# Optimization experiments

Measured on AMD Instinct MI355X. Metric: run time of the kernel, lower is better.

The kernel has to match this reference:

```python
import jax, jax.numpy as jnp
import numpy as np

H = 8  # head_num

def setup_inputs() -> dict:
    key = jax.random.key(0)
    k1, k2, k3, k4, k5 = jax.random.split(key, 5)
    n, e = 4096, 128
    x = jax.random.normal(k1, (n, e), dtype=jnp.float32)
    # torch Linear weights stored here as [in, out]; scale ~ 1/sqrt(fan_in)
    w_qkv = jax.random.normal(k2, (e, e * 3 * H), dtype=jnp.float32) * (1.0 / np.sqrt(e))
    b_qkv = jax.random.normal(k3, (e * 3 * H,), dtype=jnp.float32) * 0.01
    w_proj = jax.random.normal(k4, (e * H, e), dtype=jnp.float32) * (1.0 / np.sqrt(e * H))
    b_proj = jax.random.normal(k5, (e,), dtype=jnp.float32) * 0.01
    return {"x": x, "w_qkv": w_qkv, "b_qkv": b_qkv, "w_proj": w_proj, "b_proj": b_proj}

def reference(x, w_qkv, b_qkv, w_proj, b_proj):
    n, e = x.shape
    # packed layout along output dim is (h, d, qkv) per rearrange 'n (h d qkv) -> qkv h n d'
    qkv = (x @ w_qkv + b_qkv).reshape(n, H, e, 3)          # [n, h, d, 3]
    q = jnp.transpose(qkv[..., 0], (1, 0, 2))              # [h, n, d]
    k = jnp.transpose(qkv[..., 1], (1, 0, 2))
    v = jnp.transpose(qkv[..., 2], (1, 0, 2))
    energy = jnp.einsum('hqd,hkd->hqk', q, k)              # [h, n, n]
    scaling = jnp.asarray(e, x.dtype) ** 0.5
    att = jax.nn.softmax(energy, axis=-1) / scaling        # post-softmax scale (as in source)
    out = jnp.einsum('hqk,hkd->hqd', att, v)               # [h, n, d]
    out = jnp.transpose(out, (1, 0, 2)).reshape(n, H * e)  # [n, h*d]
    return out @ w_proj + b_proj
```

## Files before the change

### kernel.cpp

```cpp
#include <hip/hip_runtime.h>
#include <hip/hip_fp16.h>


#define N_TOK 4096
#define DH 128
#define NH 8

#define EXP2F(x) __builtin_amdgcn_exp2f(x)

typedef _Float16 f16;
typedef __attribute__((ext_vector_type(8))) _Float16 f16x8;
typedef __attribute__((ext_vector_type(2))) __fp16 hf2;
typedef __attribute__((ext_vector_type(4))) float f32x4;

#define GLD16(gsrc, ldst) __builtin_amdgcn_global_load_lds( \
    (const __attribute__((address_space(1))) void*)(gsrc), \
    (__attribute__((address_space(3))) void*)(ldst), 16, 0, 0)

__global__ __launch_bounds__(256) void conv_weights(
    const float* __restrict__ w_proj, const float* __restrict__ w_qkv,
    const float* __restrict__ b_qkv,
    f16* __restrict__ wpT, f16* __restrict__ wqkvT, float* __restrict__ bperm)
{
  int t = blockIdx.x * 256 + threadIdx.x;
  if (t < 131072) {
    int k = t >> 7, col = t & 127;
    wpT[col * 1024 + k] = (f16)w_proj[t];
  } else {
    t -= 131072;
    int k = t / 3072;
    int col = t - k * 3072;
    int hh = col / 384;
    int rem = col - hh * 384;
    int d = rem / 3;
    int s = rem - d * 3;
    int colp = s * 1024 + hh * 128 + d;
    float scale = (s == 0) ? 1.4426950408889634f : 1.0f;
    wqkvT[colp * 128 + k] = (f16)(w_qkv[t] * scale);
    if (k == 0) bperm[colp] = b_qkv[col] * scale;
  }
}

__global__ __launch_bounds__(256) void qkv_gemm2(
    const float* __restrict__ x, const f16* __restrict__ wqkvT,
    const float* __restrict__ bperm,
    f16* __restrict__ Qh, f16* __restrict__ Kh, f16* __restrict__ Vt)
{
  const int cb = blockIdx.x;
  const int rb = blockIdx.y;
  const int tid = threadIdx.x;
  const int w = tid >> 6, lane = tid & 63;
  const int l16 = lane & 15, lhi = lane >> 4;
  const int s = cb >> 3, h = cb & 7;

  f16x8 xf[2][4];
#pragma unroll
  for (int m = 0; m < 2; ++m)
#pragma unroll
    for (int kt = 0; kt < 4; ++kt) {
      const float* xp = x + (size_t)(rb * 128 + w * 32 + m * 16 + l16) * 128 + kt * 32 + lhi * 8;
      f32x4 x0 = *(const f32x4*)xp, x1 = *(const f32x4*)(xp + 4);
      f16x8 v;
#pragma unroll
      for (int j = 0; j < 4; ++j) { v[j] = (f16)x0[j]; v[4 + j] = (f16)x1[j]; }
      xf[m][kt] = v;
    }

  f32x4 acc[8][2];
#pragma unroll
  for (int nt = 0; nt < 8; ++nt)
#pragma unroll
    for (int m = 0; m < 2; ++m) acc[nt][m] = (f32x4){0.f, 0.f, 0.f, 0.f};

#pragma unroll
  for (int nt = 0; nt < 8; ++nt)
#pragma unroll
    for (int kt = 0; kt < 4; ++kt) {
      f16x8 wf = *(const f16x8*)(wqkvT + (size_t)(cb * 128 + nt * 16 + l16) * 128 + kt * 32 + lhi * 8);
      acc[nt][0] = __builtin_amdgcn_mfma_f32_16x16x32_f16(wf, xf[0][kt], acc[nt][0], 0, 0, 0);
      acc[nt][1] = __builtin_amdgcn_mfma_f32_16x16x32_f16(wf, xf[1][kt], acc[nt][1], 0, 0, 0);
    }

#pragma unroll
  for (int nt = 0; nt < 8; ++nt) {
    f32x4 bb = *(const f32x4*)(bperm + cb * 128 + nt * 16 + 4 * lhi);
#pragma unroll
    for (int m = 0; m < 2; ++m) acc[nt][m] += bb;
  }

  if (s == 2) {
#pragma unroll
    for (int nt = 0; nt < 8; ++nt)
#pragma unroll
      for (int m = 0; m < 2; ++m)
#pragma unroll
        for (int r = 0; r < 4; ++r)
          Vt[(size_t)(h * 128 + nt * 16 + 4 * lhi + r) * N_TOK + rb * 128 + w * 32 + m * 16 + l16] =
              (f16)acc[nt][m][r];
  } else {
    __shared__ f16 tr[128][136];
#pragma unroll
    for (int nt = 0; nt < 8; ++nt)
#pragma unroll
      for (int m = 0; m < 2; ++m)
#pragma unroll
        for (int r = 0; r < 4; ++r)
          tr[w * 32 + m * 16 + l16][nt * 16 + 4 * lhi + r] = (f16)acc[nt][m][r];
    __syncthreads();
    f16* dst = (s == 0 ? Qh : Kh) + (size_t)(h * N_TOK + rb * 128) * 128;
    int r = tid >> 1, dh = (tid & 1) * 64;
#pragma unroll
    for (int i = 0; i < 8; ++i)
      *(f16x8*)(dst + r * 128 + dh + i * 8) = *(const f16x8*)(&tr[r][dh + i * 8]);
  }
}

__global__ __launch_bounds__(256, 3) void flash_attn(
    const f16* __restrict__ Qh, const f16* __restrict__ Kh,
    const f16* __restrict__ Vt, f16* __restrict__ opart, float* __restrict__ mlpart)
{
  const int bid = blockIdx.x;
  const int h = bid & 7;
  const int rem8 = bid >> 3;
  const int sp = rem8 % 3, qb = rem8 / 3;
  const int tid = threadIdx.x;
  const int w = tid >> 6, lane = tid & 63;
  const int l16 = lane & 15, lhi = lane >> 4;

  __shared__ __align__(16) char smem[32768];

  f16x8 qf[2][4];
#pragma unroll
  for (int m = 0; m < 2; ++m)
#pragma unroll
    for (int kt = 0; kt < 4; ++kt)
      qf[m][kt] = *(const f16x8*)(Qh +
          (size_t)(h * N_TOK + qb * 128 + w * 32 + m * 16 + l16) * DH + kt * 32 + lhi * 8);

  int koff[4][4], voff[2][8];
#pragma unroll
  for (int nt = 0; nt < 4; ++nt) {
    int row = 32 * (nt >> 1) + 8 * (l16 >> 2) + 4 * (nt & 1) + (l16 & 3);
    int fk = (row & 3) | ((row & 8) >> 1);
#pragma unroll
    for (int kt = 0; kt < 4; ++kt)
      koff[nt][kt] = row * 256 + ((kt * 4 + lhi) ^ fk) * 16;
  }
#pragma unroll
  for (int ks = 0; ks < 2; ++ks)
#pragma unroll
    for (int dt = 0; dt < 8; ++dt) {
      int rowv = dt * 16 + l16;
      voff[ks][dt] = rowv * 128 + (((ks * 4 + lhi) ^ (rowv & 7))) * 16;
    }

  f32x4 o[2][8];
#pragma unroll
  for (int m = 0; m < 2; ++m)
#pragma unroll
    for (int dt = 0; dt < 8; ++dt) o[m][dt] = (f32x4){0.f, 0.f, 0.f, 0.f};
  float mrun[2] = {-3e38f, -3e38f}, lrun[2] = {0.f, 0.f};

  const f16* Kgh = Kh + (size_t)h * N_TOK * DH;
  const f16* Vgh = Vt + (size_t)h * DH * N_TOK;

  auto stage = [&](int kb) {
    char* kd = smem;
    char* vd = smem + 16384;
#pragma unroll
    for (int c4 = 0; c4 < 4; ++c4) {
      int c = w * 4 + c4;
      {
        int row = c * 4 + (lane >> 4);
        int fk = (row & 3) | ((row & 8) >> 1);
        const f16* src = Kgh + (size_t)(kb * 64 + row) * DH + ((lane & 15) ^ fk) * 8;
        GLD16(src, kd + c * 1024);
      }
      {
        int row = c * 8 + (lane >> 3);
        const f16* src = Vgh + (size_t)row * N_TOK + kb * 64 + ((lane & 7) ^ (row & 7)) * 8;
        GLD16(src, vd + c * 1024);
      }
    }
  };

  const int kb0 = (sp * 64) / 3;
  const int kb1 = ((sp + 1) * 64) / 3;
  const char* kd = smem;
  const char* vd = smem + 16384;

  for (int kb = kb0; kb < kb1; ++kb) {
    stage(kb);
    __syncthreads();

    f32x4 sv[2][4];
    __builtin_amdgcn_s_setprio(1);
#pragma unroll
    for (int nt = 0; nt < 4; ++nt) {
      f32x4 a0 = {0.f, 0.f, 0.f, 0.f}, a1 = {0.f, 0.f, 0.f, 0.f};
#pragma unroll
      for (int kt = 0; kt < 4; ++kt) {
        f16x8 kf = *(const f16x8*)(kd + koff[nt][kt]);
        a0 = __builtin_amdgcn_mfma_f32_16x16x32_f16(kf, qf[0][kt], a0, 0, 0, 0);
        a1 = __builtin_amdgcn_mfma_f32_16x16x32_f16(kf, qf[1][kt], a1, 0, 0, 0);
      }
      sv[0][nt] = a0; sv[1][nt] = a1;
    }
    __builtin_amdgcn_s_setprio(0);

    f16x8 pf[2][2];
#pragma unroll
    for (int m = 0; m < 2; ++m) {
      f32x4 mv;
#pragma unroll
      for (int r = 0; r < 4; ++r)
        mv[r] = fmaxf(fmaxf(sv[m][0][r], sv[m][1][r]), fmaxf(sv[m][2][r], sv[m][3][r]));
      float pmax = fmaxf(fmaxf(mv[0], mv[1]), fmaxf(mv[2], mv[3]));
      if (!__all(pmax - mrun[m] <= 8.f)) {
        float rm = fmaxf(pmax, __shfl_xor(pmax, 16));
        rm = fmaxf(rm, __shfl_xor(rm, 32));
        float mnew = fmaxf(mrun[m], rm);
        float sc = EXP2F(mrun[m] - mnew);
        lrun[m] *= sc;
#pragma unroll
        for (int dt = 0; dt < 8; ++dt) o[m][dt] *= sc;
        mrun[m] = mnew;
      }
      float mr = mrun[m];
      f32x4 ps = {0.f, 0.f, 0.f, 0.f};
#pragma unroll
      for (int nt = 0; nt < 4; ++nt)
#pragma unroll
        for (int r = 0; r < 4; ++r) {
          float p = EXP2F(sv[m][nt][r] - mr);
          sv[m][nt][r] = p;
          ps[r] += p;
        }
      lrun[m] += (ps[0] + ps[1]) + (ps[2] + ps[3]);
#pragma unroll
      for (int ks = 0; ks < 2; ++ks) {
        union { f16x8 v; hf2 hh[4]; } u;
        u.hh[0] = __builtin_amdgcn_cvt_pkrtz(sv[m][2 * ks][0], sv[m][2 * ks][1]);
        u.hh[1] = __builtin_amdgcn_cvt_pkrtz(sv[m][2 * ks][2], sv[m][2 * ks][3]);
        u.hh[2] = __builtin_amdgcn_cvt_pkrtz(sv[m][2 * ks + 1][0], sv[m][2 * ks + 1][1]);
        u.hh[3] = __builtin_amdgcn_cvt_pkrtz(sv[m][2 * ks + 1][2], sv[m][2 * ks + 1][3]);
        pf[m][ks] = u.v;
      }
    }

    __builtin_amdgcn_s_setprio(1);
#pragma unroll
    for (int ks = 0; ks < 2; ++ks)
#pragma unroll
      for (int dt = 0; dt < 8; ++dt) {
        f16x8 vf = *(const f16x8*)(vd + voff[ks][dt]);
        o[0][dt] = __builtin_amdgcn_mfma_f32_16x16x32_f16(vf, pf[0][ks], o[0][dt], 0, 0, 0);
        o[1][dt] = __builtin_amdgcn_mfma_f32_16x16x32_f16(vf, pf[1][ks], o[1][dt], 0, 0, 0);
      }
    __builtin_amdgcn_s_setprio(0);

    __syncthreads();
  }

  f16* ob = opart + ((size_t)((sp * 8 + h) * 32 + qb)) * 16384;
  float* mlb = mlpart + ((size_t)((sp * 8 + h) * 32 + qb)) * 256;
#pragma unroll
  for (int m = 0; m < 2; ++m) {
    float lr = lrun[m];
    lr += __shfl_xor(lr, 16);
    lr += __shfl_xor(lr, 32);
    float rl = 1.0f / lr;
#pragma unroll
    for (int dt = 0; dt < 8; ++dt)
#pragma unroll
      for (int r = 0; r < 4; ++r)
        ob[(dt * 16 + 4 * lhi + r) * 128 + w * 32 + m * 16 + l16] = (f16)(o[m][dt][r] * rl);
    if (lhi == 0) {
      mlb[w * 32 + m * 16 + l16] = mrun[m];
      mlb[128 + w * 32 + m * 16 + l16] = lr;
    }
  }
}

__global__ __launch_bounds__(256) void proj_combine(
    const f16* __restrict__ opart, const float* __restrict__ mlpart,
    const f16* __restrict__ wpT, const float* __restrict__ b_proj,
    float* __restrict__ out)
{
  const int tid = threadIdx.x;
  const int w = tid >> 6;
  const int lane = tid & 63;
  const int l16 = lane & 15, lhi = lane >> 4;
  const int rb = blockIdx.x * 16;
  const int qb = rb >> 7;
  const int nl0 = rb & 127;

  __shared__ f16 A[16][1032];
  __shared__ float wl[8][16][3];
  __shared__ float red[4][16][128];

  const float isc = 0.08838834764831845f;
  if (tid < 128) {
    int hh = tid >> 4, n = tid & 15;
    float mi[3], li[3];
#pragma unroll
    for (int i = 0; i < 3; ++i) {
      const float* ml = mlpart + ((size_t)((i * 8 + hh) * 32 + qb)) * 256 + nl0 + n;
      mi[i] = ml[0]; li[i] = ml[128];
    }
    float mt = fmaxf(fmaxf(mi[0], mi[1]), mi[2]);
    float ni[3], tot = 0.f;
#pragma unroll
    for (int i = 0; i < 3; ++i) { ni[i] = EXP2F(mi[i] - mt) * li[i]; tot += ni[i]; }
    float rl = isc / tot;
#pragma unroll
    for (int i = 0; i < 3; ++i) wl[hh][n][i] = ni[i] * rl;
  }
  __syncthreads();

  {
    int d = tid >> 1, nn = (tid & 1) * 8;
#pragma unroll
    for (int hh = 0; hh < 8; ++hh) {
      float sum[8] = {};
#pragma unroll
      for (int i = 0; i < 3; ++i) {
        const f16* Oi = opart + ((size_t)((i * 8 + hh) * 32 + qb)) * 16384 + d * 128 + nl0 + nn;
        f16x8 a = *(const f16x8*)Oi;
#pragma unroll
        for (int j = 0; j < 8; ++j) sum[j] += (float)a[j] * wl[hh][nn + j][i];
      }
#pragma unroll
      for (int j = 0; j < 8; ++j) A[nn + j][hh * 128 + d] = (f16)sum[j];
    }
  }
  __syncthreads();

  f32x4 o[8];
#pragma unroll
  for (int dt = 0; dt < 8; ++dt) o[dt] = (f32x4){0.f, 0.f, 0.f, 0.f};

#pragma unroll
  for (int kb = 0; kb < 8; ++kb) {
    int k0 = w * 256 + kb * 32 + lhi * 8;
    f16x8 a = *(const f16x8*)(&A[l16][k0]);
#pragma unroll
    for (int dt = 0; dt < 8; ++dt) {
      f16x8 b = *(const f16x8*)(wpT + (size_t)(dt * 16 + l16) * 1024 + k0);
      o[dt] = __builtin_amdgcn_mfma_f32_16x16x32_f16(a, b, o[dt], 0, 0, 0);
    }
  }

#pragma unroll
  for (int dt = 0; dt < 8; ++dt)
#pragma unroll
    for (int r = 0; r < 4; ++r)
      red[w][lhi * 4 + r][dt * 16 + l16] = o[dt][r];
  __syncthreads();
#pragma unroll
  for (int i = 0; i < 8; ++i) {
    int idx = tid + 256 * i;
    int row = idx >> 7, col = idx & 127;
    float v = red[0][row][col] + red[1][row][col] + red[2][row][col]
            + red[3][row][col] + b_proj[col];
    out[(size_t)(rb + row) * 128 + col] = v;
  }
}

extern "C" void kernel_launch(void* const* d_in, const int* in_sizes, int n_in,
                              void* d_out, int out_size, void* d_ws, size_t ws_size,
                              hipStream_t stream) {
  const float* x      = (const float*)d_in[0];
  const float* w_qkv  = (const float*)d_in[1];
  const float* b_qkv  = (const float*)d_in[2];
  const float* w_proj = (const float*)d_in[3];
  const float* b_proj = (const float*)d_in[4];
  float* out = (float*)d_out;

  char* ws = (char*)d_ws;
  const size_t MB = 1024 * 1024;
  f16*   Qh     = (f16*)(ws);
  f16*   Kh     = (f16*)(ws + 8 * MB);
  f16*   Vt     = (f16*)(ws + 16 * MB);
  f16*   opart  = (f16*)(ws + 24 * MB);
  float* mlpart = (float*)(ws + 48 * MB);
  f16*   wpT    = (f16*)(ws + 49 * MB);
  f16*   wqkvT  = (f16*)(ws + 49 * MB + 256 * 1024);
  float* bperm  = (float*)(ws + 50 * MB);

  hipLaunchKernelGGL(conv_weights, dim3(2048), dim3(256), 0, stream,
                     w_proj, w_qkv, b_qkv, wpT, wqkvT, bperm);
  hipLaunchKernelGGL(qkv_gemm2, dim3(24, 32), dim3(256), 0, stream,
                     x, wqkvT, bperm, Qh, Kh, Vt);
  hipLaunchKernelGGL(flash_attn, dim3(768), dim3(256), 0, stream,
                     Qh, Kh, Vt, opart, mlpart);
  hipLaunchKernelGGL(proj_combine, dim3(256), dim3(256), 0, stream,
                     opart, mlpart, wpT, b_proj, out);
}
```

Measured before the change: 136.5 us.

## Double-buffer K tiles and split V staging to overlap loads with compute

Splits K and V staging, double-buffers K in LDS so the next K tile is prefetched while the current QK^T and softmax run, and waits on V only before the PV MFMAs using vmcnt counters and raw s_barrier. Also packs the LDS offsets as pairs of 16-bit values to cut register use. This aims to hide global-to-LDS latency, but it raises LDS per block to 48KB, which may reduce how many blocks fit per CU at launch bounds of 3. It also relies on hand-written waitcnt values being correct.

```diff
diff --git a/kernel.cpp b/kernel.cpp
--- a/kernel.cpp
+++ b/kernel.cpp
@@ -127,7 +127,7 @@
   const int w = tid >> 6, lane = tid & 63;
   const int l16 = lane & 15, lhi = lane >> 4;
 
-  __shared__ __align__(16) char smem[32768];
+  __shared__ __align__(16) char smem[49152];
 
   f16x8 qf[2][4];
 #pragma unroll
@@ -137,21 +137,26 @@
       qf[m][kt] = *(const f16x8*)(Qh +
           (size_t)(h * N_TOK + qb * 128 + w * 32 + m * 16 + l16) * DH + kt * 32 + lhi * 8);
 
-  int koff[4][4], voff[2][8];
+  int koffp[8], voffp[8];
 #pragma unroll
   for (int nt = 0; nt < 4; ++nt) {
     int row = 32 * (nt >> 1) + 8 * (l16 >> 2) + 4 * (nt & 1) + (l16 & 3);
     int fk = (row & 3) | ((row & 8) >> 1);
-#pragma unroll
-    for (int kt = 0; kt < 4; ++kt)
-      koff[nt][kt] = row * 256 + ((kt * 4 + lhi) ^ fk) * 16;
+    int k0 = row * 256 + ((0 + lhi) ^ fk) * 16;
+    int k1 = row * 256 + ((4 + lhi) ^ fk) * 16;
+    int k2 = row * 256 + ((8 + lhi) ^ fk) * 16;
+    int k3 = row * 256 + ((12 + lhi) ^ fk) * 16;
+    koffp[nt * 2 + 0] = k0 | (k1 << 16);
+    koffp[nt * 2 + 1] = k2 | (k3 << 16);
   }
 #pragma unroll
   for (int ks = 0; ks < 2; ++ks)
 #pragma unroll
-    for (int dt = 0; dt < 8; ++dt) {
-      int rowv = dt * 16 + l16;
-      voff[ks][dt] = rowv * 128 + (((ks * 4 + lhi) ^ (rowv & 7))) * 16;
+    for (int d2 = 0; d2 < 4; ++d2) {
+      int r0 = (d2 * 2) * 16 + l16, r1 = (d2 * 2 + 1) * 16 + l16;
+      int v0 = r0 * 128 + (((ks * 4 + lhi) ^ (r0 & 7)) * 16);
+      int v1 = r1 * 128 + (((ks * 4 + lhi) ^ (r1 & 7)) * 16);
+      voffp[ks * 4 + d2] = v0 | (v1 << 16);
     }
 
   f32x4 o[2][8];
@@ -164,34 +169,44 @@
   const f16* Kgh = Kh + (size_t)h * N_TOK * DH;
   const f16* Vgh = Vt + (size_t)h * DH * N_TOK;
 
-  auto stage = [&](int kb) {
-    char* kd = smem;
-    char* vd = smem + 16384;
+  auto stageK = [&](int buf, int kb) {
+    char* kd = smem + buf * 16384;
 #pragma unroll
     for (int c4 = 0; c4 < 4; ++c4) {
       int c = w * 4 + c4;
-      {
-        int row = c * 4 + (lane >> 4);
-        int fk = (row & 3) | ((row & 8) >> 1);
-        const f16* src = Kgh + (size_t)(kb * 64 + row) * DH + ((lane & 15) ^ fk) * 8;
-        GLD16(src, kd + c * 1024);
-      }
-      {
-        int row = c * 8 + (lane >> 3);
-        const f16* src = Vgh + (size_t)row * N_TOK + kb * 64 + ((lane & 7) ^ (row & 7)) * 8;
-        GLD16(src, vd + c * 1024);
-      }
+      int row = c * 4 + (lane >> 4);
+      int fk = (row & 3) | ((row & 8) >> 1);
+      const f16* src = Kgh + (size_t)(kb * 64 + row) * DH + ((lane & 15) ^ fk) * 8;
+      GLD16(src, kd + c * 1024);
+    }
+  };
+  auto stageV = [&](int kb) {
+    char* vd = smem + 32768;
+#pragma unroll
+    for (int c4 = 0; c4 < 4; ++c4) {
+      int c = w * 4 + c4;
+      int row = c * 8 + (lane >> 3);
+      const f16* src = Vgh + (size_t)row * N_TOK + kb * 64 + ((lane & 7) ^ (row & 7)) * 8;
+      GLD16(src, vd + c * 1024);
     }
   };
 
   const int kb0 = (sp * 64) / 3;
   const int kb1 = ((sp + 1) * 64) / 3;
-  const char* kd = smem;
-  const char* vd = smem + 16384;
+  const char* vd = smem + 32768;
+
+  stageK(0, kb0);
+  int p = 0;
 
   for (int kb = kb0; kb < kb1; ++kb) {
-    stage(kb);
-    __syncthreads();
+    stageV(kb);
+    int nk = (kb + 1 < kb1) ? kb + 1 : kb1 - 1;
+    stageK(p ^ 1, nk);
+    asm volatile("s_waitcnt vmcnt(8)" ::: "memory");
+    __builtin_amdgcn_sched_barrier(0);
+    __builtin_amdgcn_s_barrier();
+
+    const char* kd = smem + p * 16384;
 
     f32x4 sv[2][4];
     __builtin_amdgcn_s_setprio(1);
@@ -200,7 +215,9 @@
       f32x4 a0 = {0.f, 0.f, 0.f, 0.f}, a1 = {0.f, 0.f, 0.f, 0.f};
 #pragma unroll
       for (int kt = 0; kt < 4; ++kt) {
-        f16x8 kf = *(const f16x8*)(kd + koff[nt][kt]);
+        int ko = (kt & 1) ? (int)((unsigned)koffp[nt * 2 + (kt >> 1)] >> 16)
+                          : (koffp[nt * 2 + (kt >> 1)] & 0xffff);
+        f16x8 kf = *(const f16x8*)(kd + ko);
         a0 = __builtin_amdgcn_mfma_f32_16x16x32_f16(kf, qf[0][kt], a0, 0, 0, 0);
         a1 = __builtin_amdgcn_mfma_f32_16x16x32_f16(kf, qf[1][kt], a1, 0, 0, 0);
       }
@@ -232,9 +249,9 @@
       for (int nt = 0; nt < 4; ++nt)
 #pragma unroll
         for (int r = 0; r < 4; ++r) {
-          float p = EXP2F(sv[m][nt][r] - mr);
-          sv[m][nt][r] = p;
-          ps[r] += p;
+          float pv = EXP2F(sv[m][nt][r] - mr);
+          sv[m][nt][r] = pv;
+          ps[r] += pv;
         }
       lrun[m] += (ps[0] + ps[1]) + (ps[2] + ps[3]);
 #pragma unroll
@@ -248,18 +265,25 @@
       }
     }
 
+    asm volatile("s_waitcnt vmcnt(4)" ::: "memory");
+    __builtin_amdgcn_sched_barrier(0);
+    __builtin_amdgcn_s_barrier();
+
     __builtin_amdgcn_s_setprio(1);
 #pragma unroll
     for (int ks = 0; ks < 2; ++ks)
 #pragma unroll
       for (int dt = 0; dt < 8; ++dt) {
-        f16x8 vf = *(const f16x8*)(vd + voff[ks][dt]);
+        int vo = (dt & 1) ? (int)((unsigned)voffp[ks * 4 + (dt >> 1)] >> 16)
+                          : (voffp[ks * 4 + (dt >> 1)] & 0xffff);
+        f16x8 vf = *(const f16x8*)(vd + vo);
         o[0][dt] = __builtin_amdgcn_mfma_f32_16x16x32_f16(vf, pf[0][ks], o[0][dt], 0, 0, 0);
         o[1][dt] = __builtin_amdgcn_mfma_f32_16x16x32_f16(vf, pf[1][ks], o[1][dt], 0, 0, 0);
       }
     __builtin_amdgcn_s_setprio(0);
 
-    __syncthreads();
+    __builtin_amdgcn_s_barrier();
+    p ^= 1;
   }
 
   f16* ob = opart + ((size_t)((sp * 8 + h) * 32 + qb)) * 16384;
```

Result: slower. 175.3 us (+28.5%).

## Pre-convert x to fp16 and store attention partials row-major for vector access

Applied to the files above, without the earlier changes.

Converts x to fp16 once in the weight conversion kernel so the QKV GEMM loads f16 directly instead of re-converting fp32 x in each of its 24 column blocks. Changes the opart layout from d-major to token-major so flash_attn writes packed 4-element f16 stores via cvt_pkrtz, and proj_combine reads contiguous 8-wide vectors per token row when merging the three splits. This reduces redundant global traffic and scattered scalar stores, but adds an extra pass over x and switches the output conversion to round-toward-zero.

```diff
diff --git a/kernel.cpp b/kernel.cpp
--- a/kernel.cpp
+++ b/kernel.cpp
@@ -11,6 +11,7 @@
 typedef _Float16 f16;
 typedef __attribute__((ext_vector_type(8))) _Float16 f16x8;
 typedef __attribute__((ext_vector_type(2))) __fp16 hf2;
+typedef __attribute__((ext_vector_type(4))) __fp16 hf4;
 typedef __attribute__((ext_vector_type(4))) float f32x4;
 
 #define GLD16(gsrc, ldst) __builtin_amdgcn_global_load_lds( \
@@ -19,14 +20,15 @@
 
 __global__ __launch_bounds__(256) void conv_weights(
     const float* __restrict__ w_proj, const float* __restrict__ w_qkv,
-    const float* __restrict__ b_qkv,
-    f16* __restrict__ wpT, f16* __restrict__ wqkvT, float* __restrict__ bperm)
+    const float* __restrict__ b_qkv, const float* __restrict__ x,
+    f16* __restrict__ wpT, f16* __restrict__ wqkvT, float* __restrict__ bperm,
+    f16* __restrict__ xh)
 {
   int t = blockIdx.x * 256 + threadIdx.x;
   if (t < 131072) {
     int k = t >> 7, col = t & 127;
     wpT[col * 1024 + k] = (f16)w_proj[t];
-  } else {
+  } else if (t < 524288) {
     t -= 131072;
     int k = t / 3072;
     int col = t - k * 3072;
@@ -38,11 +40,14 @@
     float scale = (s == 0) ? 1.4426950408889634f : 1.0f;
     wqkvT[colp * 128 + k] = (f16)(w_qkv[t] * scale);
     if (k == 0) bperm[colp] = b_qkv[col] * scale;
+  } else {
+    t -= 524288;
+    xh[t] = (f16)x[t];
   }
 }
 
 __global__ __launch_bounds__(256) void qkv_gemm2(
-    const float* __restrict__ x, const f16* __restrict__ wqkvT,
+    const f16* __restrict__ xh, const f16* __restrict__ wqkvT,
     const float* __restrict__ bperm,
     f16* __restrict__ Qh, f16* __restrict__ Kh, f16* __restrict__ Vt)
 {
@@ -57,14 +62,9 @@
 #pragma unroll
   for (int m = 0; m < 2; ++m)
 #pragma unroll
-    for (int kt = 0; kt < 4; ++kt) {
-      const float* xp = x + (size_t)(rb * 128 + w * 32 + m * 16 + l16) * 128 + kt * 32 + lhi * 8;
-      f32x4 x0 = *(const f32x4*)xp, x1 = *(const f32x4*)(xp + 4);
-      f16x8 v;
-#pragma unroll
-      for (int j = 0; j < 4; ++j) { v[j] = (f16)x0[j]; v[4 + j] = (f16)x1[j]; }
-      xf[m][kt] = v;
-    }
+    for (int kt = 0; kt < 4; ++kt)
+      xf[m][kt] = *(const f16x8*)(xh +
+          (size_t)(rb * 128 + w * 32 + m * 16 + l16) * 128 + kt * 32 + lhi * 8);
 
   f32x4 acc[8][2];
 #pragma unroll
@@ -270,14 +270,17 @@
     lr += __shfl_xor(lr, 16);
     lr += __shfl_xor(lr, 32);
     float rl = 1.0f / lr;
-#pragma unroll
-    for (int dt = 0; dt < 8; ++dt)
-#pragma unroll
-      for (int r = 0; r < 4; ++r)
-        ob[(dt * 16 + 4 * lhi + r) * 128 + w * 32 + m * 16 + l16] = (f16)(o[m][dt][r] * rl);
+    int n = w * 32 + m * 16 + l16;
+#pragma unroll
+    for (int dt = 0; dt < 8; ++dt) {
+      union { hf4 v; hf2 h[2]; } u;
+      u.h[0] = __builtin_amdgcn_cvt_pkrtz(o[m][dt][0] * rl, o[m][dt][1] * rl);
+      u.h[1] = __builtin_amdgcn_cvt_pkrtz(o[m][dt][2] * rl, o[m][dt][3] * rl);
+      *(hf4*)(ob + (size_t)n * 128 + dt * 16 + 4 * lhi) = u.v;
+    }
     if (lhi == 0) {
-      mlb[w * 32 + m * 16 + l16] = mrun[m];
-      mlb[128 + w * 32 + m * 16 + l16] = lr;
+      mlb[n] = mrun[m];
+      mlb[128 + n] = lr;
     }
   }
 }
@@ -319,19 +322,23 @@
   __syncthreads();
 
   {
-    int d = tid >> 1, nn = (tid & 1) * 8;
-#pragma unroll
-    for (int hh = 0; hh < 8; ++hh) {
-      float sum[8] = {};
-#pragma unroll
-      for (int i = 0; i < 3; ++i) {
-        const f16* Oi = opart + ((size_t)((i * 8 + hh) * 32 + qb)) * 16384 + d * 128 + nl0 + nn;
-        f16x8 a = *(const f16x8*)Oi;
-#pragma unroll
-        for (int j = 0; j < 8; ++j) sum[j] += (float)a[j] * wl[hh][nn + j][i];
-      }
-#pragma unroll
-      for (int j = 0; j < 8; ++j) A[nn + j][hh * 128 + d] = (f16)sum[j];
+    int n = tid & 15, c = tid >> 4;
+    int hh = c >> 1, d0 = (c & 1) * 64;
+    size_t roff = (size_t)(nl0 + n) * 128 + d0;
+    const f16* O0 = opart + ((size_t)((0 + hh) * 32 + qb)) * 16384 + roff;
+    const f16* O1 = opart + ((size_t)((8 + hh) * 32 + qb)) * 16384 + roff;
+    const f16* O2 = opart + ((size_t)((16 + hh) * 32 + qb)) * 16384 + roff;
+    float w0 = wl[hh][n][0], w1 = wl[hh][n][1], w2 = wl[hh][n][2];
+#pragma unroll
+    for (int j = 0; j < 8; ++j) {
+      f16x8 a0 = *(const f16x8*)(O0 + j * 8);
+      f16x8 a1 = *(const f16x8*)(O1 + j * 8);
+      f16x8 a2 = *(const f16x8*)(O2 + j * 8);
+      f16x8 res;
+#pragma unroll
+      for (int e = 0; e < 8; ++e)
+        res[e] = (f16)((float)a0[e] * w0 + (float)a1[e] * w1 + (float)a2[e] * w2);
+      *(f16x8*)(&A[n][hh * 128 + d0 + j * 8]) = res;
     }
   }
   __syncthreads();
@@ -387,11 +394,12 @@
   f16*   wpT    = (f16*)(ws + 49 * MB);
   f16*   wqkvT  = (f16*)(ws + 49 * MB + 256 * 1024);
   float* bperm  = (float*)(ws + 50 * MB);
-
-  hipLaunchKernelGGL(conv_weights, dim3(2048), dim3(256), 0, stream,
-                     w_proj, w_qkv, b_qkv, wpT, wqkvT, bperm);
+  f16*   xh     = (f16*)(ws + 50 * MB + 256 * 1024);
+
+  hipLaunchKernelGGL(conv_weights, dim3(4096), dim3(256), 0, stream,
+                     w_proj, w_qkv, b_qkv, x, wpT, wqkvT, bperm, xh);
   hipLaunchKernelGGL(qkv_gemm2, dim3(24, 32), dim3(256), 0, stream,
-                     x, wqkvT, bperm, Qh, Kh, Vt);
+                     xh, wqkvT, bperm, Qh, Kh, Vt);
   hipLaunchKernelGGL(flash_attn, dim3(768), dim3(256), 0, stream,
                      Qh, Kh, Vt, opart, mlpart);
   hipLaunchKernelGGL(proj_combine, dim3(256), dim3(256), 0, stream,
```

Measured after the change: 129.3 us. -5.2%, faster.
